# Kernel optimization log

Measured on AMD Instinct MI355X. Metric: run time of the kernel, lower is better.

## Reference

```python
import jax, jax.numpy as jnp
import numpy as np

D_MODEL = 272
D_STATE = 32
N_LAYERS = 12
D_INNER = 2 * D_MODEL      # expand=2 (mamba_ssm default)
D_CONV = 4                 # mamba_ssm default
DT_RANK = (D_MODEL + 15) // 16  # ceil(272/16) = 17
B_SZ = 2
SEQ = 512


def setup_inputs() -> dict:
    key = jax.random.key(0)
    ks = jax.random.split(key, 16)
    rn = lambda k, shape, s=0.02: jax.random.normal(k, shape, jnp.float32) * s
    # dt bias init: softplus^{-1} of dt in [1e-3, 0.1] (mamba-style)
    dt0 = jax.random.uniform(ks[6], (N_LAYERS, 2, D_INNER), jnp.float32, 1e-3, 0.1)
    a_log = jnp.broadcast_to(jnp.log(jnp.arange(1, D_STATE + 1, dtype=jnp.float32)),
                             (N_LAYERS, 2, D_INNER, D_STATE))
    return {
        "x": jax.random.normal(ks[0], (B_SZ, SEQ, D_MODEL), jnp.float32),
        "y": jax.random.uniform(ks[1], (B_SZ, 1), jnp.float32),
        "in_proj_w": rn(ks[2], (N_LAYERS, 2, 2 * D_INNER, D_MODEL)),
        "conv_w": rn(ks[3], (N_LAYERS, 2, D_INNER, D_CONV), 0.1),
        "conv_b": jnp.zeros((N_LAYERS, 2, D_INNER), jnp.float32),
        "x_proj_w": rn(ks[4], (N_LAYERS, 2, DT_RANK + 2 * D_STATE, D_INNER)),
        "dt_proj_w": rn(ks[5], (N_LAYERS, 2, D_INNER, DT_RANK), 0.1),
        "dt_proj_b": jnp.log(jnp.expm1(dt0)),
        "A_log": a_log,
        "Dskip": jnp.ones((N_LAYERS, 2, D_INNER), jnp.float32),
        "out_proj_w": rn(ks[7], (N_LAYERS, 2, D_MODEL, D_INNER)),
        "lambda_q1": rn(ks[8], (N_LAYERS, D_MODEL), 0.05),
        "norm1_w": jnp.ones((N_LAYERS, D_MODEL), jnp.float32),
        "norm2_w": jnp.ones((N_LAYERS, D_MODEL), jnp.float32),
        "mlp_w": rn(ks[9], (D_MODEL, D_MODEL)),
        "mlp_b": jnp.zeros((D_MODEL,), jnp.float32),
        "predict_w": rn(ks[10], (1, D_MODEL + 1)),
        "predict_b": jnp.zeros((1,), jnp.float32),
    }


def _rmsnorm(x, w, eps=1e-5):
    return x * jax.lax.rsqrt(jnp.mean(x * x, axis=-1, keepdims=True) + eps) * w


def _mamba(x, p):
    """Single-direction Mamba block. x: (B, L, D_MODEL)."""
    in_w, cw, cb, xw, dtw, dtb, a_log, dskip, ow = p
    bsz = x.shape[0]
    xz = jnp.einsum('bld,ed->ble', x, in_w)            # (B,L,2*D_INNER)
    xin, z = jnp.split(xz, 2, axis=-1)
    # causal depthwise conv1d, kernel 4
    xc = jax.lax.conv_general_dilated(
        xin.transpose(0, 2, 1), cw[:, None, :], (1,), [(D_CONV - 1, 0)],
        feature_group_count=D_INNER, dimension_numbers=('NCL', 'OIL', 'NCL'))
    xc = jax.nn.silu(xc + cb[:, None]).transpose(0, 2, 1)  # (B,L,D_INNER)
    dbc = jnp.einsum('bld,ed->ble', xc, xw)
    dt, Bm, Cm = jnp.split(dbc, [DT_RANK, DT_RANK + D_STATE], axis=-1)
    dt = jax.nn.softplus(jnp.einsum('blr,dr->bld', dt, dtw) + dtb)  # (B,L,D_INNER)
    A = -jnp.exp(a_log)                                  # (D_INNER, D_STATE)

    @jax.checkpoint
    def step(h, inp):
        dt_t, x_t, B_t, C_t = inp                        # (B,Din),(B,Din),(B,Ds),(B,Ds)
        h = jnp.exp(dt_t[..., None] * A) * h + (dt_t * x_t)[..., None] * B_t[:, None, :]
        return h, jnp.einsum('bds,bs->bd', h, C_t)

    h0 = jnp.zeros((bsz, D_INNER, D_STATE), x.dtype)
    xs = (dt.transpose(1, 0, 2), xc.transpose(1, 0, 2),
          Bm.transpose(1, 0, 2), Cm.transpose(1, 0, 2))
    _, ys = jax.lax.scan(step, h0, xs)                   # ys: (L,B,D_INNER)
    yo = ys.transpose(1, 0, 2) + dskip * xc
    yo = yo * jax.nn.silu(z)
    return jnp.einsum('bld,od->blo', yo, ow)


def _forward(x, y, in_proj_w, conv_w, conv_b, x_proj_w, dt_proj_w, dt_proj_b,
             A_log, Dskip, out_proj_w, lambda_q1, norm1_w, norm2_w,
             mlp_w, mlp_b, predict_w, predict_b):
    mats = (in_proj_w, conv_w, conv_b, x_proj_w, dt_proj_w, dt_proj_b, A_log, Dskip, out_proj_w)
    for i in range(N_LAYERS):
        lam_init = 0.8 - 0.6 * np.exp(-0.3 * i)
        xn = _rmsnorm(x, norm1_w[i])
        lam_full = jax.nn.sigmoid(jnp.sum(lambda_q1[i])) + lam_init
        y1 = _mamba(xn, tuple(a[i, 0] for a in mats))
        y2 = jnp.flip(_mamba(jnp.flip(xn, 1), tuple(a[i, 1] for a in mats)), 1)
        attn = _rmsnorm(y1 - lam_full * y2, norm2_w[i])
        x = x + attn * (1.0 - lam_init)
    x2 = jax.nn.relu(jnp.mean(x, axis=1) @ mlp_w.T + mlp_b)
    feats = jnp.concatenate([x2, y], axis=-1)
    logits = feats @ predict_w.T + predict_b
    return logits, x2


def reference(x, y, in_proj_w, conv_w, conv_b, x_proj_w, dt_proj_w, dt_proj_b,
              A_log, Dskip, out_proj_w, lambda_q1, norm1_w, norm2_w,
              mlp_w, mlp_b, predict_w, predict_b):
    return _forward(x, y, in_proj_w, conv_w, conv_b, x_proj_w, dt_proj_w, dt_proj_b,
                    A_log, Dskip, out_proj_w, lambda_q1, norm1_w, norm2_w,
                    mlp_w, mlp_b, predict_w, predict_b)
```

## Files before the change

kernel.cpp:

```cpp
#include <hip/hip_runtime.h>
#include <math.h>

#define DM   272
#define DS   32
#define DI   544
#define DTR  17
#define SEQL 512
#define NB   2
#define ROWS 1024
#define DXZ  1088
#define NL   12

#define OFF_X     0
#define OFF_INVR  278528
#define OFF_XZ    279552
#define OFF_XCT   2507776
#define OFF_DTT   3621888
#define OFF_ZT    4736000
#define OFF_BM    5850112
#define OFF_CM    5915648
#define OFF_YOT   5981184
#define OFF_Y12   7095296
#define OFF_XMP   7652352
#define OFF_DTWT  7656704

__device__ __forceinline__ float sigmoid_fast(float x){ return 1.f/(1.f+__expf(-x)); }
__device__ __forceinline__ float softplus_f(float x){ return (x > 20.f) ? x : log1pf(__expf(x)); }

__device__ __forceinline__ float block_reduce_256(float v, volatile float* sred, int tid){
#pragma unroll
  for (int m=32; m>=1; m>>=1) v += __shfl_xor(v, m);
  __syncthreads();
  if ((tid & 63) == 0) sred[tid>>6] = v;
  __syncthreads();
  return sred[0]+sred[1]+sred[2]+sred[3];
}

__global__ __launch_bounds__(64) void k_init(const float* __restrict__ x0,
                                             float* __restrict__ xb, float* __restrict__ invr){
  int r = blockIdx.x, tid = threadIdx.x;
  float ss = 0.f;
  for (int c=tid; c<DM; c+=64){ float v = x0[(size_t)r*DM+c]; xb[(size_t)r*DM+c]=v; ss += v*v; }
#pragma unroll
  for (int m=32;m>=1;m>>=1) ss += __shfl_xor(ss,m);
  if (tid==0) invr[r] = rsqrtf(ss*(1.f/DM)+1e-5f);
}

__global__ __launch_bounds__(256) void k_transpose(const float* __restrict__ dtw,
                                                   float* __restrict__ dtwT){
  int idx = blockIdx.x*256 + threadIdx.x;
  const int T2 = 24*544*DTR;
  if (idx < T2){
    int ld = idx / (544*DTR); int rem = idx - ld*(544*DTR);
    int d = rem / DTR; int r = rem - d*DTR;
    dtwT[(size_t)ld*DTR*544 + (size_t)r*544 + d] = dtw[idx];
  }
}

__global__ __launch_bounds__(256) void k_inproj(
    const float* __restrict__ xb, const float* __restrict__ invr,
    const float* __restrict__ n1w, const float* __restrict__ inw,
    float* __restrict__ xz)
{
  __shared__ float As[16][76];
  __shared__ float Bs[16][76];
  const int tid = threadIdx.x;
  const int m0 = blockIdx.x << 6;
  const int nt = blockIdx.y;
  const int dir = (nt >= 17) ? 1 : 0;
  const int n0l = (nt - dir*17) << 6;
  const float* wb = inw + (size_t)(dir*1088 + n0l)*272;
  const int tr = tid & 15, tc = tid >> 4;
  const int lr = tid >> 2, lk = (tid & 3) << 2;
  const float ivr = invr[m0 + lr];
  const float* xrow = xb + (size_t)(m0 + lr)*272;
  const float* wrow = wb + (size_t)lr*272;
  float acc[4][4];
#pragma unroll
  for (int i=0;i<4;i++)
#pragma unroll
    for (int j=0;j<4;j++) acc[i][j]=0.f;
  for (int k0=0;k0<272;k0+=16){
    float4 a4 = *(const float4*)(xrow + k0 + lk);
    float4 g4 = *(const float4*)(n1w + k0 + lk);
    float4 b4 = *(const float4*)(wrow + k0 + lk);
    As[lk+0][lr] = a4.x*ivr*g4.x;
    As[lk+1][lr] = a4.y*ivr*g4.y;
    As[lk+2][lr] = a4.z*ivr*g4.z;
    As[lk+3][lr] = a4.w*ivr*g4.w;
    Bs[lk+0][lr] = b4.x; Bs[lk+1][lr]=b4.y; Bs[lk+2][lr]=b4.z; Bs[lk+3][lr]=b4.w;
    __syncthreads();
#pragma unroll
    for (int kk=0;kk<16;kk++){
      float4 av = *(const float4*)(&As[kk][tr<<2]);
      float4 bv = *(const float4*)(&Bs[kk][tc<<2]);
      acc[0][0]+=av.x*bv.x; acc[0][1]+=av.x*bv.y; acc[0][2]+=av.x*bv.z; acc[0][3]+=av.x*bv.w;
      acc[1][0]+=av.y*bv.x; acc[1][1]+=av.y*bv.y; acc[1][2]+=av.y*bv.z; acc[1][3]+=av.y*bv.w;
      acc[2][0]+=av.z*bv.x; acc[2][1]+=av.z*bv.y; acc[2][2]+=av.z*bv.z; acc[2][3]+=av.z*bv.w;
      acc[3][0]+=av.w*bv.x; acc[3][1]+=av.w*bv.y; acc[3][2]+=av.w*bv.z; acc[3][3]+=av.w*bv.w;
    }
    __syncthreads();
  }
#pragma unroll
  for (int i=0;i<4;i++){
    int r = m0 + (tr<<2) + i;
    int b = r >> 9, t = r & 511;
    int ts = dir ? (511 - t) : t;
    float4 v = make_float4(acc[i][0],acc[i][1],acc[i][2],acc[i][3]);
    *(float4*)(xz + (size_t)((dir*NB + b)*SEQL + ts)*DXZ + n0l + (tc<<2)) = v;
  }
}

__global__ __launch_bounds__(512) void k_xdt(
  const float* __restrict__ xz, const float* __restrict__ cwl, const float* __restrict__ cbl,
  const float* __restrict__ xwl, const float* __restrict__ dtwTl, const float* __restrict__ dtbl,
  float* __restrict__ xcT, float* __restrict__ dtT, float* __restrict__ zT,
  float* __restrict__ Bmg, float* __restrict__ Cmg)
{
  __shared__ float xcs[8][548];
  __shared__ float part[8][8][82];
  __shared__ float dts[8][DTR];
  const int tid = threadIdx.x;
  const int blk = blockIdx.x;
  const int seg = blk >> 6;
  const int dir = seg >> 1;
  const int t0 = (blk & 63) << 3;
  const float* xzb  = xz + (size_t)seg*SEQL*DXZ;
  const float* cw   = cwl + dir*DI*4;
  const float* cb   = cbl + dir*DI;
  const float* xw   = xwl + (size_t)dir*81*DI;
  const float* dtwT = dtwTl + (size_t)dir*DTR*DI;
  const float* dtb  = dtbl + dir*DI;
  const size_t chb = (size_t)seg*DI;

  for (int j = tid; j < DI; j += 512){
    float4 w4 = *(const float4*)(cw + j*4);
    float bj = cb[j];
    float xv[11];
#pragma unroll
    for (int q=0; q<11; q++){
      int t = t0 + q - 3;
      xv[q] = (t >= 0) ? xzb[(size_t)t*DXZ + j] : 0.f;
    }
    float xo[8], zo[8];
#pragma unroll
    for (int rr=0; rr<8; rr++){
      float acc = bj + w4.x*xv[rr] + w4.y*xv[rr+1] + w4.z*xv[rr+2] + w4.w*xv[rr+3];
      float v = acc * sigmoid_fast(acc);
      xcs[rr][j] = v; xo[rr] = v;
      zo[rr] = xzb[(size_t)(t0+rr)*DXZ + 544 + j];
    }
    float* xr = xcT + (chb + j)*SEQL + t0;
    *(float4*)(xr)   = make_float4(xo[0],xo[1],xo[2],xo[3]);
    *(float4*)(xr+4) = make_float4(xo[4],xo[5],xo[6],xo[7]);
    float* zr = zT + (chb + j)*SEQL + t0;
    *(float4*)(zr)   = make_float4(zo[0],zo[1],zo[2],zo[3]);
    *(float4*)(zr+4) = make_float4(zo[4],zo[5],zo[6],zo[7]);
  }
  __syncthreads();

  if (tid < 328){
    const int i = tid >> 3, ks = tid & 7;
    const int e0 = 2*i;
    const int e1r = (e0+1 < 81) ? (e0+1) : 80;
    const int kb = ks*68;
    const float* w0 = xw + (size_t)e0*DI + kb;
    const float* w1 = xw + (size_t)e1r*DI + kb;
    float acc0[8], acc1[8];
#pragma unroll
    for (int rr=0; rr<8; rr++){ acc0[rr]=0.f; acc1[rr]=0.f; }
    for (int k=0; k<68; k+=4){
      float4 wa = *(const float4*)(w0 + k);
      float4 wb = *(const float4*)(w1 + k);
#pragma unroll
      for (int rr=0; rr<8; rr++){
        float4 x4 = *(const float4*)(&xcs[rr][kb + k]);
        acc0[rr] = fmaf(wa.x,x4.x, fmaf(wa.y,x4.y, fmaf(wa.z,x4.z, fmaf(wa.w,x4.w, acc0[rr]))));
        acc1[rr] = fmaf(wb.x,x4.x, fmaf(wb.y,x4.y, fmaf(wb.z,x4.z, fmaf(wb.w,x4.w, acc1[rr]))));
      }
    }
#pragma unroll
    for (int rr=0; rr<8; rr++){
      part[ks][rr][e0]   = acc0[rr];
      part[ks][rr][e0+1] = acc1[rr];
    }
  }
  __syncthreads();

  for (int idx=tid; idx<648; idx+=512){
    int ta = idx / 81, e = idx - ta*81;
    float s = 0.f;
#pragma unroll
    for (int ks=0; ks<8; ks++) s += part[ks][ta][e];
    size_t row = (size_t)seg*SEQL + t0 + ta;
    if (e < DTR)      dts[ta][e] = s;
    else if (e < 49)  Bmg[row*DS + (e-DTR)] = s;
    else              Cmg[row*DS + (e-49)] = s;
  }
  __syncthreads();

  {
    const int c1 = tid;
    const bool h2 = tid < 32; const int c2 = 512 + tid;
    float w1[DTR], w2[DTR];
#pragma unroll
    for (int q=0; q<DTR; q++){
      w1[q] = dtwT[q*DI + c1];
      w2[q] = h2 ? dtwT[q*DI + c2] : 0.f;
    }
    float b1 = dtb[c1], b2 = h2 ? dtb[c2] : 0.f;
    float o1[8], o2[8];
#pragma unroll
    for (int rr=0; rr<8; rr++){
      float a1=b1, a2=b2;
#pragma unroll
      for (int q=0; q<DTR; q++){
        float dv = dts[rr][q];
        a1 = fmaf(w1[q],dv,a1); a2 = fmaf(w2[q],dv,a2);
      }
      o1[rr]=softplus_f(a1); o2[rr]=softplus_f(a2);
    }
    float* r1 = dtT + (chb + c1)*SEQL + t0;
    *(float4*)(r1)   = make_float4(o1[0],o1[1],o1[2],o1[3]);
    *(float4*)(r1+4) = make_float4(o1[4],o1[5],o1[6],o1[7]);
    if (h2){
      float* r2 = dtT + (chb + c2)*SEQL + t0;
      *(float4*)(r2)   = make_float4(o2[0],o2[1],o2[2],o2[3]);
      *(float4*)(r2+4) = make_float4(o2[4],o2[5],o2[6],o2[7]);
    }
  }
}

__global__ __launch_bounds__(128) void k_scan(
  const float* __restrict__ dtT, const float* __restrict__ xcT,
  const float* __restrict__ Bmg, const float* __restrict__ Cmg,
  const float* __restrict__ alogl, const float* __restrict__ dskl,
  const float* __restrict__ zT, float* __restrict__ yoT)
{
  __shared__ float hl[16][33], pl[16][33], Hi[16][33];
  const int d = blockIdx.x, b = blockIdx.y, dir = blockIdx.z;
  const int seg = dir*NB + b;
  const int tid = threadIdx.x;
  const int c = tid >> 3, sg = tid & 7, s0 = sg << 2;
  float A0,A1,A2,A3;
  {
    const float* al = alogl + (size_t)(dir*DI + d)*DS + s0;
    A0 = -expf(al[0]); A1 = -expf(al[1]); A2 = -expf(al[2]); A3 = -expf(al[3]);
  }
  const size_t cr = ((size_t)seg*DI + d)*SEQL;
  const float* dtr = dtT + cr;
  const float* xcr = xcT + cr;
  const float* zr  = zT  + cr;
  float* yor = yoT + cr;
  const float* Bp = Bmg + (size_t)seg*SEQL*DS + s0;
  const float* Cp = Cmg + (size_t)seg*SEQL*DS + s0;
  float h0=0,h1=0,h2=0,h3=0,p0=1,p1=1,p2=1,p3=1;
  const int tb = c << 5;
  for (int tq=0; tq<8; tq++){
    const int t4 = tb + (tq<<2);
    float4 dt4 = *(const float4*)(dtr + t4);
    const float* dtp4 = (const float*)&dt4;
    float4 xc4 = *(const float4*)(xcr + t4);
    const float* xcp4 = (const float*)&xc4;
#pragma unroll
    for (int u=0; u<4; u++){
      float ldt = dtp4[u], lxc = xcp4[u];
      float4 B4 = *(const float4*)(Bp + (size_t)(t4+u)*DS);
      float uu = ldt*lxc;
      float e;
      e = __expf(ldt*A0); h0 = fmaf(e,h0,uu*B4.x); p0*=e;
      e = __expf(ldt*A1); h1 = fmaf(e,h1,uu*B4.y); p1*=e;
      e = __expf(ldt*A2); h2 = fmaf(e,h2,uu*B4.z); p2*=e;
      e = __expf(ldt*A3); h3 = fmaf(e,h3,uu*B4.w); p3*=e;
    }
  }
  hl[c][s0]=h0; hl[c][s0+1]=h1; hl[c][s0+2]=h2; hl[c][s0+3]=h3;
  pl[c][s0]=p0; pl[c][s0+1]=p1; pl[c][s0+2]=p2; pl[c][s0+3]=p3;
  __syncthreads();
  if (tid < 32){
    float H = 0.f;
    Hi[0][tid] = 0.f;
    for (int cc=1; cc<16; cc++){
      H = fmaf(pl[cc-1][tid], H, hl[cc-1][tid]);
      Hi[cc][tid] = H;
    }
  }
  __syncthreads();
  h0=Hi[c][s0]; h1=Hi[c][s0+1]; h2=Hi[c][s0+2]; h3=Hi[c][s0+3];
  const float dsk = dskl[dir*DI + d];
  for (int tq=0; tq<8; tq++){
    const int t4 = tb + (tq<<2);
    float4 dt4 = *(const float4*)(dtr + t4);
    const float* dtp4 = (const float*)&dt4;
    float4 xc4 = *(const float4*)(xcr + t4);
    const float* xcp4 = (const float*)&xc4;
    float4 z4 = *(const float4*)(zr + t4);
    const float* zp4 = (const float*)&z4;
    float yv[4];
#pragma unroll
    for (int u=0; u<4; u++){
      float ldt = dtp4[u], lxc = xcp4[u];
      float4 B4 = *(const float4*)(Bp + (size_t)(t4+u)*DS);
      float4 C4 = *(const float4*)(Cp + (size_t)(t4+u)*DS);
      float uu = ldt*lxc;
      float e;
      e = __expf(ldt*A0); h0 = fmaf(e,h0,uu*B4.x);
      e = __expf(ldt*A1); h1 = fmaf(e,h1,uu*B4.y);
      e = __expf(ldt*A2); h2 = fmaf(e,h2,uu*B4.z);
      e = __expf(ldt*A3); h3 = fmaf(e,h3,uu*B4.w);
      float y = h0*C4.x + h1*C4.y + h2*C4.z + h3*C4.w;
      y += __shfl_xor(y,1); y += __shfl_xor(y,2); y += __shfl_xor(y,4);
      float z = zp4[u];
      yv[u] = fmaf(dsk, lxc, y) * (z * sigmoid_fast(z));
    }
    if (sg==0) *(float4*)(yor + t4) = make_float4(yv[0],yv[1],yv[2],yv[3]);
  }
}

__global__ __launch_bounds__(128) void k_outproj(
    const float* __restrict__ yoT, const float* __restrict__ ow, float* __restrict__ y12)
{
  __shared__ float As[16][68];
  __shared__ float Bs[16][40];
  const int tid = threadIdx.x;
  const int m0 = blockIdx.x << 6;
  const int n0 = blockIdx.y << 5;
  const int dir = blockIdx.z;
  const int bseg = m0 >> 9;
  const int t0 = m0 & 511;
  const float* At = yoT + (size_t)(dir*NB + bseg)*DI*SEQL;
  const float* W = ow + (size_t)dir*DM*DI;
  const int smi = (tid & 15) << 2;
  const int skk = tid >> 4;
  const int lrb = tid >> 2, lkb = (tid & 3) << 2;
  const int tr = tid & 15, tc = tid >> 4;
  const int nb = n0 + lrb;
  const bool bvalid = nb < DM;
  const float* wrow = W + (size_t)(bvalid ? nb : 0)*DI;
  float acc[4][4];
#pragma unroll
  for (int i=0;i<4;i++)
#pragma unroll
    for (int j=0;j<4;j++) acc[i][j]=0.f;
  for (int k0=0;k0<544;k0+=16){
    float4 a0 = *(const float4*)(At + (size_t)(k0+skk)*SEQL + t0 + smi);
    float4 a1 = *(const float4*)(At + (size_t)(k0+skk+8)*SEQL + t0 + smi);
    *(float4*)(&As[skk][smi])   = a0;
    *(float4*)(&As[skk+8][smi]) = a1;
    float4 b4 = bvalid ? *(const float4*)(wrow + k0 + lkb) : make_float4(0.f,0.f,0.f,0.f);
    Bs[lkb+0][lrb]=b4.x; Bs[lkb+1][lrb]=b4.y; Bs[lkb+2][lrb]=b4.z; Bs[lkb+3][lrb]=b4.w;
    __syncthreads();
#pragma unroll
    for (int kk=0;kk<16;kk++){
      float4 av = *(const float4*)(&As[kk][tr<<2]);
      float4 bv = *(const float4*)(&Bs[kk][tc<<2]);
      acc[0][0]+=av.x*bv.x; acc[0][1]+=av.x*bv.y; acc[0][2]+=av.x*bv.z; acc[0][3]+=av.x*bv.w;
      acc[1][0]+=av.y*bv.x; acc[1][1]+=av.y*bv.y; acc[1][2]+=av.y*bv.z; acc[1][3]+=av.y*bv.w;
      acc[2][0]+=av.z*bv.x; acc[2][1]+=av.z*bv.y; acc[2][2]+=av.z*bv.z; acc[2][3]+=av.z*bv.w;
      acc[3][0]+=av.w*bv.x; acc[3][1]+=av.w*bv.y; acc[3][2]+=av.w*bv.z; acc[3][3]+=av.w*bv.w;
    }
    __syncthreads();
  }
  int col = n0 + (tc<<2);
  if (col < DM){
#pragma unroll
    for (int i=0;i<4;i++){
      int r = m0 + (tr<<2) + i;
      int b = r >> 9, t = r & 511;
      int ts = dir ? (511 - t) : t;
      float4 v = make_float4(acc[i][0],acc[i][1],acc[i][2],acc[i][3]);
      *(float4*)(y12 + (size_t)dir*ROWS*DM + (size_t)(b*SEQL+ts)*DM + col) = v;
    }
  }
}

__global__ __launch_bounds__(256) void k_combine(
  const float* __restrict__ y12, const float* __restrict__ lamq,
  const float* __restrict__ n2w, float* __restrict__ xb,
  float* __restrict__ invr, float lam_init, float omli)
{
  __shared__ float sred[4];
  const int tid = threadIdx.x;
  const int r = blockIdx.x;
  const float* y1 = y12 + (size_t)r*DM;
  const float* y2 = y12 + (size_t)ROWS*DM + (size_t)r*DM;
  float lp = lamq[tid];
  if (tid < 16) lp += lamq[tid+256];
  float lsum = block_reduce_256(lp, sred, tid);
  float lam = sigmoid_fast(lsum) + lam_init;
  float a0 = y1[tid] - lam*y2[tid];
  float a1 = 0.f;
  if (tid<16) a1 = y1[tid+256] - lam*y2[tid+256];
  float ss = block_reduce_256(a0*a0 + a1*a1, sred, tid);
  float rms = rsqrtf(ss*(1.f/DM) + 1e-5f);
  float xo0 = xb[(size_t)r*DM + tid] + a0*rms*n2w[tid]*omli;
  float xo1 = 0.f;
  if (tid<16) xo1 = xb[(size_t)r*DM + tid+256] + a1*rms*n2w[tid+256]*omli;
  xb[(size_t)r*DM+tid] = xo0;
  if (tid<16) xb[(size_t)r*DM+tid+256] = xo1;
  float ss2 = block_reduce_256(xo0*xo0 + xo1*xo1, sred, tid);
  if (tid==0) invr[r] = rsqrtf(ss2*(1.f/DM) + 1e-5f);
}

__global__ __launch_bounds__(256) void k_head1(const float* __restrict__ xb, float* __restrict__ xmp){
  int ch = blockIdx.x, b = blockIdx.y, tid = threadIdx.x;
  int t0 = ch*64;
  float s0=0.f, s1=0.f;
  for (int t=t0; t<t0+64; t++){
    const float* row = xb + (size_t)(b*SEQL+t)*DM;
    s0 += row[tid];
    if (tid<16) s1 += row[tid+256];
  }
  xmp[(size_t)(b*8+ch)*DM + tid] = s0;
  if (tid<16) xmp[(size_t)(b*8+ch)*DM + tid+256] = s1;
}

__global__ __launch_bounds__(256) void k_head2(
  const float* __restrict__ xmp, const float* __restrict__ yin,
  const float* __restrict__ mlpw, const float* __restrict__ mlpb,
  const float* __restrict__ pw, const float* __restrict__ pb,
  float* __restrict__ out)
{
  __shared__ float xm[2][DM];
  __shared__ float x2s[2][DM];
  __shared__ float sred[4];
  int tid = threadIdx.x;
  for (int idx=tid; idx<2*DM; idx+=256){
    int b = idx / DM, c = idx - b*DM;
    float s=0.f;
    for (int ch=0; ch<8; ch++) s += xmp[(size_t)(b*8+ch)*DM + c];
    xm[b][c] = s * (1.f/SEQL);
  }
  __syncthreads();
  for (int idx=tid; idx<2*DM; idx+=256){
    int b = idx / DM, c = idx - b*DM;
    float acc = mlpb[c];
    const float* wr = mlpw + (size_t)c*DM;
    for (int k=0;k<DM;k++) acc += wr[k]*xm[b][k];
    float v = fmaxf(acc, 0.f);
    x2s[b][c] = v;
    out[2 + b*DM + c] = v;
  }
  __syncthreads();
  for (int b=0;b<2;b++){
    float p = x2s[b][tid]*pw[tid];
    if (tid<16) p += x2s[b][tid+256]*pw[tid+256];
    float tot = block_reduce_256(p, sred, tid);
    if (tid==0) out[b] = tot + yin[b]*pw[DM] + pb[0];
  }
}

extern "C" void kernel_launch(void* const* d_in, const int* in_sizes, int n_in,
                              void* d_out, int out_size, void* d_ws, size_t ws_size,
                              hipStream_t stream)
{
  const float* x0     = (const float*)d_in[0];
  const float* yin    = (const float*)d_in[1];
  const float* in_w   = (const float*)d_in[2];
  const float* conv_w = (const float*)d_in[3];
  const float* conv_b = (const float*)d_in[4];
  const float* x_w    = (const float*)d_in[5];
  const float* dt_w   = (const float*)d_in[6];
  const float* dt_b   = (const float*)d_in[7];
  const float* a_log  = (const float*)d_in[8];
  const float* dskip  = (const float*)d_in[9];
  const float* out_w  = (const float*)d_in[10];
  const float* lamq   = (const float*)d_in[11];
  const float* n1w    = (const float*)d_in[12];
  const float* n2w    = (const float*)d_in[13];
  const float* mlpw   = (const float*)d_in[14];
  const float* mlpb   = (const float*)d_in[15];
  const float* pw     = (const float*)d_in[16];
  const float* pb     = (const float*)d_in[17];

  float* ws  = (float*)d_ws;
  float* xb  = ws + OFF_X;
  float* invr= ws + OFF_INVR;
  float* xz  = ws + OFF_XZ;
  float* xcT = ws + OFF_XCT;
  float* dtT = ws + OFF_DTT;
  float* zT  = ws + OFF_ZT;
  float* Bm  = ws + OFF_BM;
  float* Cm  = ws + OFF_CM;
  float* yoT = ws + OFF_YOT;
  float* y12 = ws + OFF_Y12;
  float* xmp = ws + OFF_XMP;
  float* dtwT= ws + OFF_DTWT;
  float* outp = (float*)d_out;

  k_transpose<<<(24*544*DTR + 255)/256, 256, 0, stream>>>(dt_w, dtwT);
  k_init<<<ROWS, 64, 0, stream>>>(x0, xb, invr);
  for (int i=0;i<NL;i++){
    float lam_init = 0.8f - 0.6f*expf(-0.3f*(float)i);
    k_inproj<<<dim3(16,34), 256, 0, stream>>>(xb, invr, n1w + (size_t)i*DM,
        in_w + (size_t)i*2176*272, xz);
    k_xdt<<<256, 512, 0, stream>>>(xz,
        conv_w + (size_t)i*2*DI*4, conv_b + (size_t)i*2*DI,
        x_w + (size_t)i*2*81*DI, dtwT + (size_t)i*2*DTR*DI, dt_b + (size_t)i*2*DI,
        xcT, dtT, zT, Bm, Cm);
    k_scan<<<dim3(DI,NB,2), 128, 0, stream>>>(dtT, xcT, Bm, Cm,
        a_log + (size_t)i*2*DI*DS, dskip + (size_t)i*2*DI, zT, yoT);
    k_outproj<<<dim3(16,9,2), 128, 0, stream>>>(yoT, out_w + (size_t)i*2*DM*DI, y12);
    k_combine<<<ROWS, 256, 0, stream>>>(y12, lamq + (size_t)i*DM, n2w + (size_t)i*DM,
        xb, invr, lam_init, 1.f - lam_init);
  }
  k_head1<<<dim3(8,2), 256, 0, stream>>>(xb, xmp);
  k_head2<<<1, 256, 0, stream>>>(xmp, yin, mlpw, mlpb, pw, pb, outp);
}
```

Baseline: 1.630 ms.

## Run in/out projections on bf16x3 split-precision MFMA instead of FP32 SIMT GEMMs

```diff
diff --git a/kernel.cpp b/kernel.cpp
--- a/kernel.cpp
+++ b/kernel.cpp
@@ -10,9 +10,13 @@
 #define ROWS 1024
 #define DXZ  1088
 #define NL   12
+#define KP   288
+
+typedef unsigned short ushort_t;
+typedef __attribute__((ext_vector_type(8))) short bx8;
+typedef __attribute__((ext_vector_type(4))) float fx4;
 
 #define OFF_X     0
-#define OFF_INVR  278528
 #define OFF_XZ    279552
 #define OFF_XCT   2507776
 #define OFF_DTT   3621888
@@ -23,10 +27,28 @@
 #define OFF_Y12   7095296
 #define OFF_XMP   7652352
 #define OFF_DTWT  7656704
+#define OFF_XNH   7878656
+#define OFF_XNL   8026112
+#define OFF_YTMH  8173568
+#define OFF_YTML  8730624
+#define OFF_WINH  9287680
+#define OFF_WINL  13047808
+#define OFF_WOUTH 16807936
+#define OFF_WOUTL 18583552
+
+#define NINW  (12*2176*KP)
+#define NOUTW (12*544*544)
 
 __device__ __forceinline__ float sigmoid_fast(float x){ return 1.f/(1.f+__expf(-x)); }
 __device__ __forceinline__ float softplus_f(float x){ return (x > 20.f) ? x : log1pf(__expf(x)); }
 
+__device__ __forceinline__ void bf16split(float x, ushort_t& h, ushort_t& l){
+  unsigned uh = __float_as_uint(x) & 0xffff0000u;
+  h = (ushort_t)(uh >> 16);
+  float r = x - __uint_as_float(uh);
+  l = (ushort_t)(__float_as_uint(r) >> 16);
+}
+
 __device__ __forceinline__ float block_reduce_256(float v, volatile float* sred, int tid){
 #pragma unroll
   for (int m=32; m>=1; m>>=1) v += __shfl_xor(v, m);
@@ -36,14 +58,23 @@
   return sred[0]+sred[1]+sred[2]+sred[3];
 }
 
-__global__ __launch_bounds__(64) void k_init(const float* __restrict__ x0,
-                                             float* __restrict__ xb, float* __restrict__ invr){
-  int r = blockIdx.x, tid = threadIdx.x;
-  float ss = 0.f;
-  for (int c=tid; c<DM; c+=64){ float v = x0[(size_t)r*DM+c]; xb[(size_t)r*DM+c]=v; ss += v*v; }
-#pragma unroll
-  for (int m=32;m>=1;m>>=1) ss += __shfl_xor(ss,m);
-  if (tid==0) invr[r] = rsqrtf(ss*(1.f/DM)+1e-5f);
+__global__ __launch_bounds__(256) void k_convw(const float* __restrict__ inw,
+    const float* __restrict__ outw,
+    ushort_t* __restrict__ winh, ushort_t* __restrict__ winl,
+    ushort_t* __restrict__ wouth, ushort_t* __restrict__ woutl)
+{
+  int idx = blockIdx.x*256 + threadIdx.x;
+  if (idx < NINW){
+    int k = idx % KP; int row = idx / KP;
+    float v = (k < DM) ? inw[(size_t)row*DM + k] : 0.f;
+    ushort_t h,l; bf16split(v,h,l);
+    winh[idx]=h; winl[idx]=l;
+  } else if (idx < NINW + NOUTW){
+    int j = idx - NINW;
+    float v = outw[j];
+    ushort_t h,l; bf16split(v,h,l);
+    wouth[j]=h; woutl[j]=l;
+  }
 }
 
 __global__ __launch_bounds__(256) void k_transpose(const float* __restrict__ dtw,
@@ -57,57 +88,74 @@
   }
 }
 
-__global__ __launch_bounds__(256) void k_inproj(
-    const float* __restrict__ xb, const float* __restrict__ invr,
-    const float* __restrict__ n1w, const float* __restrict__ inw,
-    float* __restrict__ xz)
-{
-  __shared__ float As[16][76];
-  __shared__ float Bs[16][76];
+__global__ __launch_bounds__(64) void k_init(const float* __restrict__ x0,
+                                             const float* __restrict__ n1w0,
+                                             float* __restrict__ xb,
+                                             ushort_t* __restrict__ xnh, ushort_t* __restrict__ xnl){
+  int r = blockIdx.x, tid = threadIdx.x;
+  float vv[5]; float ss = 0.f;
+#pragma unroll
+  for (int i=0;i<5;i++){
+    int c = tid + i*64; float v = 0.f;
+    if (c < DM){ v = x0[(size_t)r*DM+c]; xb[(size_t)r*DM+c]=v; }
+    vv[i]=v; ss += v*v;
+  }
+#pragma unroll
+  for (int m=32;m>=1;m>>=1) ss += __shfl_xor(ss,m);
+  float ivr = rsqrtf(ss*(1.f/DM)+1e-5f);
+#pragma unroll
+  for (int i=0;i<5;i++){
+    int c = tid + i*64;
+    if (c < DM){
+      ushort_t h,l; bf16split(vv[i]*ivr*n1w0[c],h,l);
+      xnh[(size_t)r*KP+c]=h; xnl[(size_t)r*KP+c]=l;
+    }
+  }
+  if (tid < 16){ xnh[(size_t)r*KP+DM+tid]=0; xnl[(size_t)r*KP+DM+tid]=0; }
+}
+
+__global__ __launch_bounds__(256) void k_gin(
+  const ushort_t* __restrict__ xnh, const ushort_t* __restrict__ xnl,
+  const ushort_t* __restrict__ wh,  const ushort_t* __restrict__ wl,
+  float* __restrict__ xz)
+{
   const int tid = threadIdx.x;
+  const int wv = tid >> 6, lane = tid & 63;
+  const int m16 = lane & 15, quad = lane >> 4;
+  const int q8 = quad << 3;
   const int m0 = blockIdx.x << 6;
   const int nt = blockIdx.y;
   const int dir = (nt >= 17) ? 1 : 0;
   const int n0l = (nt - dir*17) << 6;
-  const float* wb = inw + (size_t)(dir*1088 + n0l)*272;
-  const int tr = tid & 15, tc = tid >> 4;
-  const int lr = tid >> 2, lk = (tid & 3) << 2;
-  const float ivr = invr[m0 + lr];
-  const float* xrow = xb + (size_t)(m0 + lr)*272;
-  const float* wrow = wb + (size_t)lr*272;
-  float acc[4][4];
-#pragma unroll
-  for (int i=0;i<4;i++)
-#pragma unroll
-    for (int j=0;j<4;j++) acc[i][j]=0.f;
-  for (int k0=0;k0<272;k0+=16){
-    float4 a4 = *(const float4*)(xrow + k0 + lk);
-    float4 g4 = *(const float4*)(n1w + k0 + lk);
-    float4 b4 = *(const float4*)(wrow + k0 + lk);
-    As[lk+0][lr] = a4.x*ivr*g4.x;
-    As[lk+1][lr] = a4.y*ivr*g4.y;
-    As[lk+2][lr] = a4.z*ivr*g4.z;
-    As[lk+3][lr] = a4.w*ivr*g4.w;
-    Bs[lk+0][lr] = b4.x; Bs[lk+1][lr]=b4.y; Bs[lk+2][lr]=b4.z; Bs[lk+3][lr]=b4.w;
-    __syncthreads();
-#pragma unroll
-    for (int kk=0;kk<16;kk++){
-      float4 av = *(const float4*)(&As[kk][tr<<2]);
-      float4 bv = *(const float4*)(&Bs[kk][tc<<2]);
-      acc[0][0]+=av.x*bv.x; acc[0][1]+=av.x*bv.y; acc[0][2]+=av.x*bv.z; acc[0][3]+=av.x*bv.w;
-      acc[1][0]+=av.y*bv.x; acc[1][1]+=av.y*bv.y; acc[1][2]+=av.y*bv.z; acc[1][3]+=av.y*bv.w;
-      acc[2][0]+=av.z*bv.x; acc[2][1]+=av.z*bv.y; acc[2][2]+=av.z*bv.z; acc[2][3]+=av.z*bv.w;
-      acc[3][0]+=av.w*bv.x; acc[3][1]+=av.w*bv.y; acc[3][2]+=av.w*bv.z; acc[3][3]+=av.w*bv.w;
-    }
-    __syncthreads();
-  }
-#pragma unroll
-  for (int i=0;i<4;i++){
-    int r = m0 + (tr<<2) + i;
-    int b = r >> 9, t = r & 511;
-    int ts = dir ? (511 - t) : t;
-    float4 v = make_float4(acc[i][0],acc[i][1],acc[i][2],acc[i][3]);
-    *(float4*)(xz + (size_t)((dir*NB + b)*SEQL + ts)*DXZ + n0l + (tc<<2)) = v;
+  const int ncol = n0l + (wv<<4) + m16;
+  const ushort_t* bhp = wh + (size_t)(dir*1088 + ncol)*KP + q8;
+  const ushort_t* blp = wl + (size_t)(dir*1088 + ncol)*KP + q8;
+  const ushort_t* ahp = xnh + (size_t)(m0 + m16)*KP + q8;
+  const ushort_t* alp = xnl + (size_t)(m0 + m16)*KP + q8;
+  fx4 acc[4];
+#pragma unroll
+  for (int mt=0;mt<4;mt++) acc[mt] = (fx4){0.f,0.f,0.f,0.f};
+  for (int k0=0;k0<KP;k0+=32){
+    bx8 bh = *(const bx8*)(bhp + k0);
+    bx8 bl = *(const bx8*)(blp + k0);
+#pragma unroll
+    for (int mt=0;mt<4;mt++){
+      bx8 ah = *(const bx8*)(ahp + (size_t)mt*16*KP + k0);
+      bx8 al = *(const bx8*)(alp + (size_t)mt*16*KP + k0);
+      acc[mt] = __builtin_amdgcn_mfma_f32_16x16x32_bf16(ah, bh, acc[mt], 0,0,0);
+      acc[mt] = __builtin_amdgcn_mfma_f32_16x16x32_bf16(al, bh, acc[mt], 0,0,0);
+      acc[mt] = __builtin_amdgcn_mfma_f32_16x16x32_bf16(ah, bl, acc[mt], 0,0,0);
+    }
+  }
+#pragma unroll
+  for (int mt=0;mt<4;mt++){
+#pragma unroll
+    for (int r=0;r<4;r++){
+      int rg = m0 + mt*16 + quad*4 + r;
+      int b = rg >> 9, t = rg & 511;
+      int ts = dir ? (511 - t) : t;
+      xz[((size_t)((dir*NB + b)*SEQL + ts))*DXZ + ncol] = acc[mt][r];
+    }
   }
 }
 
@@ -317,59 +365,86 @@
   }
 }
 
-__global__ __launch_bounds__(128) void k_outproj(
-    const float* __restrict__ yoT, const float* __restrict__ ow, float* __restrict__ y12)
-{
-  __shared__ float As[16][68];
-  __shared__ float Bs[16][40];
+__global__ __launch_bounds__(256) void k_yotm(const float* __restrict__ yoT,
+                                              ushort_t* __restrict__ ytmh,
+                                              ushort_t* __restrict__ ytml){
+  __shared__ float tl[32][65];
   const int tid = threadIdx.x;
+  const int d0 = blockIdx.x << 5;
+  const int t0 = blockIdx.y << 6;
+  const int seg = blockIdx.z;
+  const int ty = tid >> 4, tx = tid & 15;
+#pragma unroll
+  for (int p=0; p<2; p++){
+    int d = p*16 + ty;
+    float4 v = *(const float4*)(yoT + ((size_t)(seg*DI + d0 + d))*SEQL + t0 + tx*4);
+    tl[d][tx*4+0]=v.x; tl[d][tx*4+1]=v.y; tl[d][tx*4+2]=v.z; tl[d][tx*4+3]=v.w;
+  }
+  __syncthreads();
+  const int tloc = tid >> 2, dq = (tid & 3) << 3;
+  ushort_t h[8], l[8];
+#pragma unroll
+  for (int j=0;j<8;j++) bf16split(tl[dq+j][tloc], h[j], l[j]);
+  uint4 ph, pl4;
+  ph.x = (unsigned)h[0] | ((unsigned)h[1]<<16);
+  ph.y = (unsigned)h[2] | ((unsigned)h[3]<<16);
+  ph.z = (unsigned)h[4] | ((unsigned)h[5]<<16);
+  ph.w = (unsigned)h[6] | ((unsigned)h[7]<<16);
+  pl4.x = (unsigned)l[0] | ((unsigned)l[1]<<16);
+  pl4.y = (unsigned)l[2] | ((unsigned)l[3]<<16);
+  pl4.z = (unsigned)l[4] | ((unsigned)l[5]<<16);
+  pl4.w = (unsigned)l[6] | ((unsigned)l[7]<<16);
+  size_t base = ((size_t)(seg*SEQL + t0 + tloc))*DI + d0 + dq;
+  *(uint4*)(ytmh + base) = ph;
+  *(uint4*)(ytml + base) = pl4;
+}
+
+__global__ __launch_bounds__(256) void k_gout(
+  const ushort_t* __restrict__ ath, const ushort_t* __restrict__ atl,
+  const ushort_t* __restrict__ wh,  const ushort_t* __restrict__ wl,
+  float* __restrict__ y12)
+{
+  const int tid = threadIdx.x;
+  const int wv = tid >> 6, lane = tid & 63;
+  const int m16 = lane & 15, quad = lane >> 4;
+  const int q8 = quad << 3;
   const int m0 = blockIdx.x << 6;
-  const int n0 = blockIdx.y << 5;
   const int dir = blockIdx.z;
+  const int nloc = (blockIdx.y << 6) + (wv<<4) + m16;
+  const bool nval = nloc < DM;
+  const int nrow = dir*DM + (nval ? nloc : (DM-1));
   const int bseg = m0 >> 9;
-  const int t0 = m0 & 511;
-  const float* At = yoT + (size_t)(dir*NB + bseg)*DI*SEQL;
-  const float* W = ow + (size_t)dir*DM*DI;
-  const int smi = (tid & 15) << 2;
-  const int skk = tid >> 4;
-  const int lrb = tid >> 2, lkb = (tid & 3) << 2;
-  const int tr = tid & 15, tc = tid >> 4;
-  const int nb = n0 + lrb;
-  const bool bvalid = nb < DM;
-  const float* wrow = W + (size_t)(bvalid ? nb : 0)*DI;
-  float acc[4][4];
-#pragma unroll
-  for (int i=0;i<4;i++)
-#pragma unroll
-    for (int j=0;j<4;j++) acc[i][j]=0.f;
-  for (int k0=0;k0<544;k0+=16){
-    float4 a0 = *(const float4*)(At + (size_t)(k0+skk)*SEQL + t0 + smi);
-    float4 a1 = *(const float4*)(At + (size_t)(k0+skk+8)*SEQL + t0 + smi);
-    *(float4*)(&As[skk][smi])   = a0;
-    *(float4*)(&As[skk+8][smi]) = a1;
-    float4 b4 = bvalid ? *(const float4*)(wrow + k0 + lkb) : make_float4(0.f,0.f,0.f,0.f);
-    Bs[lkb+0][lrb]=b4.x; Bs[lkb+1][lrb]=b4.y; Bs[lkb+2][lrb]=b4.z; Bs[lkb+3][lrb]=b4.w;
-    __syncthreads();
-#pragma unroll
-    for (int kk=0;kk<16;kk++){
-      float4 av = *(const float4*)(&As[kk][tr<<2]);
-      float4 bv = *(const float4*)(&Bs[kk][tc<<2]);
-      acc[0][0]+=av.x*bv.x; acc[0][1]+=av.x*bv.y; acc[0][2]+=av.x*bv.z; acc[0][3]+=av.x*bv.w;
-      acc[1][0]+=av.y*bv.x; acc[1][1]+=av.y*bv.y; acc[1][2]+=av.y*bv.z; acc[1][3]+=av.y*bv.w;
-      acc[2][0]+=av.z*bv.x; acc[2][1]+=av.z*bv.y; acc[2][2]+=av.z*bv.z; acc[2][3]+=av.z*bv.w;
-      acc[3][0]+=av.w*bv.x; acc[3][1]+=av.w*bv.y; acc[3][2]+=av.w*bv.z; acc[3][3]+=av.w*bv.w;
-    }
-    __syncthreads();
-  }
-  int col = n0 + (tc<<2);
-  if (col < DM){
-#pragma unroll
-    for (int i=0;i<4;i++){
-      int r = m0 + (tr<<2) + i;
-      int b = r >> 9, t = r & 511;
-      int ts = dir ? (511 - t) : t;
-      float4 v = make_float4(acc[i][0],acc[i][1],acc[i][2],acc[i][3]);
-      *(float4*)(y12 + (size_t)dir*ROWS*DM + (size_t)(b*SEQL+ts)*DM + col) = v;
+  const int tr0 = m0 & 511;
+  const int seg = dir*NB + bseg;
+  const ushort_t* bhp = wh + (size_t)nrow*DI + q8;
+  const ushort_t* blp = wl + (size_t)nrow*DI + q8;
+  const ushort_t* ahp = ath + ((size_t)(seg*SEQL) + tr0 + m16)*DI + q8;
+  const ushort_t* alp = atl + ((size_t)(seg*SEQL) + tr0 + m16)*DI + q8;
+  fx4 acc[4];
+#pragma unroll
+  for (int mt=0;mt<4;mt++) acc[mt] = (fx4){0.f,0.f,0.f,0.f};
+  for (int k0=0;k0<DI;k0+=32){
+    bx8 bh = *(const bx8*)(bhp + k0);
+    bx8 bl = *(const bx8*)(blp + k0);
+#pragma unroll
+    for (int mt=0;mt<4;mt++){
+      bx8 ah = *(const bx8*)(ahp + (size_t)mt*16*DI + k0);
+      bx8 al = *(const bx8*)(alp + (size_t)mt*16*DI + k0);
+      acc[mt] = __builtin_amdgcn_mfma_f32_16x16x32_bf16(ah, bh, acc[mt], 0,0,0);
+      acc[mt] = __builtin_amdgcn_mfma_f32_16x16x32_bf16(al, bh, acc[mt], 0,0,0);
+      acc[mt] = __builtin_amdgcn_mfma_f32_16x16x32_bf16(ah, bl, acc[mt], 0,0,0);
+    }
+  }
+  if (nval){
+#pragma unroll
+    for (int mt=0;mt<4;mt++){
+#pragma unroll
+      for (int r=0;r<4;r++){
+        int rg = m0 + mt*16 + quad*4 + r;
+        int b = rg >> 9, t = rg & 511;
+        int ts = dir ? (511 - t) : t;
+        y12[(size_t)dir*ROWS*DM + ((size_t)(b*SEQL + ts))*DM + nloc] = acc[mt][r];
+      }
     }
   }
 }
@@ -377,7 +452,8 @@
 __global__ __launch_bounds__(256) void k_combine(
   const float* __restrict__ y12, const float* __restrict__ lamq,
   const float* __restrict__ n2w, float* __restrict__ xb,
-  float* __restrict__ invr, float lam_init, float omli)
+  const float* __restrict__ n1wn, ushort_t* __restrict__ xnh, ushort_t* __restrict__ xnl,
+  float lam_init, float omli)
 {
   __shared__ float sred[4];
   const int tid = threadIdx.x;
@@ -399,7 +475,16 @@
   xb[(size_t)r*DM+tid] = xo0;
   if (tid<16) xb[(size_t)r*DM+tid+256] = xo1;
   float ss2 = block_reduce_256(xo0*xo0 + xo1*xo1, sred, tid);
-  if (tid==0) invr[r] = rsqrtf(ss2*(1.f/DM) + 1e-5f);
+  float ivn = rsqrtf(ss2*(1.f/DM) + 1e-5f);
+  {
+    ushort_t h,l; bf16split(xo0*ivn*n1wn[tid], h, l);
+    xnh[(size_t)r*KP + tid] = h; xnl[(size_t)r*KP + tid] = l;
+  }
+  if (tid < 16){
+    ushort_t h,l; bf16split(xo1*ivn*n1wn[tid+256], h, l);
+    xnh[(size_t)r*KP + tid+256] = h; xnl[(size_t)r*KP + tid+256] = l;
+    xnh[(size_t)r*KP + DM + tid] = 0; xnl[(size_t)r*KP + DM + tid] = 0;
+  }
 }
 
 __global__ __launch_bounds__(256) void k_head1(const float* __restrict__ xb, float* __restrict__ xmp){
@@ -475,7 +560,6 @@
 
   float* ws  = (float*)d_ws;
   float* xb  = ws + OFF_X;
-  float* invr= ws + OFF_INVR;
   float* xz  = ws + OFF_XZ;
   float* xcT = ws + OFF_XCT;
   float* dtT = ws + OFF_DTT;
@@ -486,23 +570,34 @@
   float* y12 = ws + OFF_Y12;
   float* xmp = ws + OFF_XMP;
   float* dtwT= ws + OFF_DTWT;
+  ushort_t* xnh  = (ushort_t*)(ws + OFF_XNH);
+  ushort_t* xnl  = (ushort_t*)(ws + OFF_XNL);
+  ushort_t* ytmh = (ushort_t*)(ws + OFF_YTMH);
+  ushort_t* ytml = (ushort_t*)(ws + OFF_YTML);
+  ushort_t* winh = (ushort_t*)(ws + OFF_WINH);
+  ushort_t* winl = (ushort_t*)(ws + OFF_WINL);
+  ushort_t* wouth= (ushort_t*)(ws + OFF_WOUTH);
+  ushort_t* woutl= (ushort_t*)(ws + OFF_WOUTL);
   float* outp = (float*)d_out;
 
+  k_convw<<<(NINW + NOUTW + 255)/256, 256, 0, stream>>>(in_w, out_w, winh, winl, wouth, woutl);
   k_transpose<<<(24*544*DTR + 255)/256, 256, 0, stream>>>(dt_w, dtwT);
-  k_init<<<ROWS, 64, 0, stream>>>(x0, xb, invr);
+  k_init<<<ROWS, 64, 0, stream>>>(x0, n1w, xb, xnh, xnl);
   for (int i=0;i<NL;i++){
     float lam_init = 0.8f - 0.6f*expf(-0.3f*(float)i);
-    k_inproj<<<dim3(16,34), 256, 0, stream>>>(xb, invr, n1w + (size_t)i*DM,
-        in_w + (size_t)i*2176*272, xz);
+    k_gin<<<dim3(16,34), 256, 0, stream>>>(xnh, xnl,
+        winh + (size_t)i*2176*KP, winl + (size_t)i*2176*KP, xz);
     k_xdt<<<256, 512, 0, stream>>>(xz,
         conv_w + (size_t)i*2*DI*4, conv_b + (size_t)i*2*DI,
         x_w + (size_t)i*2*81*DI, dtwT + (size_t)i*2*DTR*DI, dt_b + (size_t)i*2*DI,
         xcT, dtT, zT, Bm, Cm);
     k_scan<<<dim3(DI,NB,2), 128, 0, stream>>>(dtT, xcT, Bm, Cm,
         a_log + (size_t)i*2*DI*DS, dskip + (size_t)i*2*DI, zT, yoT);
-    k_outproj<<<dim3(16,9,2), 128, 0, stream>>>(yoT, out_w + (size_t)i*2*DM*DI, y12);
+    k_yotm<<<dim3(17,8,4), 256, 0, stream>>>(yoT, ytmh, ytml);
+    k_gout<<<dim3(16,5,2), 256, 0, stream>>>(ytmh, ytml,
+        wouth + (size_t)i*544*544, woutl + (size_t)i*544*544, y12);
     k_combine<<<ROWS, 256, 0, stream>>>(y12, lamq + (size_t)i*DM, n2w + (size_t)i*DM,
-        xb, invr, lam_init, 1.f - lam_init);
+        xb, n1w + (size_t)((i+1)%NL)*DM, xnh, xnl, lam_init, 1.f - lam_init);
   }
   k_head1<<<dim3(8,2), 256, 0, stream>>>(xb, xmp);
   k_head2<<<1, 256, 0, stream>>>(xmp, yin, mlpw, mlpb, pw, pb, outp);
```

Result: faster. 1.390 ms (-14.7%).
